# Kernel optimization log

Measured on AMD Instinct MI355X. Metric: run time of the kernel, lower is better.

Reference implementation:

```python
import jax, jax.numpy as jnp
import numpy as np

N = 50000
E = 400000
C_IN = 32
H = 64
RATIO = 0.5
SEQ_LEN = 5


def setup_inputs() -> dict:
    key = jax.random.key(0)
    ks = jax.random.split(key, 12)
    x = jax.random.normal(ks[0], (N, C_IN), jnp.float32)
    row = jax.random.randint(ks[1], (E,), 0, N, jnp.int32)
    off = jax.random.randint(ks[2], (E,), 1, N, jnp.int32)
    col = ((row + off) % N).astype(jnp.int32)  # no self-loops
    edge_index = jnp.stack([row, col])
    mask = jax.random.uniform(ks[3], (N,)) < 0.5

    def g(k, shape, fan):
        return jax.random.normal(k, shape, jnp.float32) / np.float32(np.sqrt(fan))

    return {
        "x": x, "edge_index": edge_index, "mask": mask,
        "conv0_w": g(ks[4], (C_IN, H), C_IN), "conv0_b": jnp.zeros((H,), jnp.float32),
        "conv1_w": g(ks[5], (H, H), H), "conv1_b": jnp.zeros((H,), jnp.float32),
        "pool_w": g(ks[6], (H,), H),
        "up_w": g(ks[7], (H, H), H), "up_b": jnp.zeros((H,), jnp.float32),
        "lstm0_w_ih": g(ks[8], (4 * H, H), H), "lstm0_w_hh": g(ks[9], (4 * H, H), H),
        "lstm0_b_ih": jnp.zeros((4 * H,), jnp.float32), "lstm0_b_hh": jnp.zeros((4 * H,), jnp.float32),
        "fin_w_ih": g(ks[10], (4 * H, H), H), "fin_w_hh": g(ks[11], (4 * H, H), H),
        "fin_b_ih": jnp.zeros((4 * H,), jnp.float32), "fin_b_hh": jnp.zeros((4 * H,), jnp.float32),
    }


def _coalesce(row, col, w, n):
    # sum duplicate (row, col) entries; output sorted by (row, col)
    key = row.astype(np.int64) * n + col.astype(np.int64)
    uk, inv = np.unique(key, return_inverse=True)
    w2 = np.bincount(inv, weights=w.astype(np.float64), minlength=uk.shape[0]).astype(np.float32)
    return uk // n, uk % n, w2


def _augment_adj(row, col, w, n):
    # remove self loops, add self loops (weight 1), compute A @ A (sparse), remove self loops
    m = row != col
    row = np.concatenate([row[m].astype(np.int64), np.arange(n, dtype=np.int64)])
    col = np.concatenate([col[m].astype(np.int64), np.arange(n, dtype=np.int64)])
    w = np.concatenate([w[m].astype(np.float32), np.ones(n, np.float32)])
    row, col, w = _coalesce(row, col, w, n)  # CSR-ordered
    cnt = np.bincount(row, minlength=n)
    indptr = np.concatenate([[0], np.cumsum(cnt)])
    dk = cnt[col]                      # out-degree of middle node k for each edge (i,k)
    starts = indptr[col]
    total = int(dk.sum())
    seg = np.repeat(np.cumsum(dk) - dk, dk)
    gi = np.repeat(starts, dk) + (np.arange(total) - seg)
    oi = np.repeat(row, dk)
    oj = col[gi]
    ow = np.repeat(w, dk) * w[gi]
    r2, c2, w2 = _coalesce(oi, oj, ow, n)
    m2 = r2 != c2
    return r2[m2], c2[m2], w2[m2]


def _gcn(x, row, col, ew, n, W, b):
    # GCNConv(improved=True): self-loop weight 2.0, symmetric deg^-1/2 normalization,
    # aggregate messages at target (col)
    h = x @ W
    loop = jnp.arange(n, dtype=row.dtype)
    r = jnp.concatenate([row, loop])
    c = jnp.concatenate([col, loop])
    w = jnp.concatenate([ew, jnp.full((n,), 2.0, ew.dtype)])
    deg = jax.ops.segment_sum(w, c, num_segments=n)
    dinv = jnp.where(deg > 0, jax.lax.rsqrt(deg), 0.0)
    norm = dinv[r] * w * dinv[c]
    out = jax.ops.segment_sum(norm[:, None] * h[r], c, num_segments=n)
    return out + b


def _sequences(x, mi):
    # sliding window [idx-L+1, idx] per masked node, zero left-padded
    t = mi[:, None] + jnp.arange(SEQ_LEN)[None, :] - (SEQ_LEN - 1)  # [M, L]
    return jnp.where((t >= 0)[:, :, None], x[jnp.clip(t, 0)], 0.0)


def _lstm_last(seq, w_ih, w_hh, b_ih, b_hh):
    # torch LSTM gate order: i, f, g, o; zero init state; return last hidden
    h = jnp.zeros((seq.shape[0], w_hh.shape[1]), seq.dtype)
    c = jnp.zeros_like(h)
    def step(carry, xt):
        h, c = carry
        g = xt @ w_ih.T + h @ w_hh.T + b_ih + b_hh
        i, f, gg, o = jnp.split(g, 4, axis=-1)
        c = jax.nn.sigmoid(f) * c + jax.nn.sigmoid(i) * jnp.tanh(gg)
        h = jax.nn.sigmoid(o) * jnp.tanh(c)
        return (h, c), None
    (h, _), _ = jax.lax.scan(step, (h, c), jnp.swapaxes(seq, 0, 1))
    return h


def reference(x, edge_index, mask, conv0_w, conv0_b, conv1_w, conv1_b, pool_w,
              up_w, up_b, lstm0_w_ih, lstm0_w_hh, lstm0_b_ih, lstm0_b_hh,
              fin_w_ih, fin_w_hh, fin_b_ih, fin_b_hh):
    n = x.shape[0]
    row0, col0 = edge_index[0], edge_index[1]
    ew0 = jnp.ones((row0.shape[0],), x.dtype)

    # down conv 0
    x1 = jax.nn.relu(_gcn(x, row0, col0, ew0, n, conv0_w, conv0_b))

    # augment_adj: sparse (A+I)^2 without diagonal (structural, constant)
    r2, c2, w2 = _augment_adj(np.asarray(row0), np.asarray(col0),
                              np.ones(row0.shape[0], np.float32), n)

    # TopKPooling: score = tanh((x.w)/||w||), keep top ceil(ratio*n)
    score = jnp.tanh((x1 @ pool_w) / jnp.linalg.norm(pool_w))
    k = int(np.ceil(RATIO * n))
    perm = np.argsort(-np.asarray(score), kind="stable")[:k]
    remap = np.full(n, -1, np.int64)
    remap[perm] = np.arange(k)
    keep = (remap[r2] >= 0) & (remap[c2] >= 0)
    pr = jnp.asarray(remap[r2[keep]].astype(np.int32))
    pc = jnp.asarray(remap[c2[keep]].astype(np.int32))
    pw = jnp.asarray(w2[keep])
    permj = jnp.asarray(perm.astype(np.int32))
    xp = x1[permj] * score[permj][:, None]

    # down conv 1 on pooled graph
    x2 = jax.nn.relu(_gcn(xp, pr, pc, pw, k, conv1_w, conv1_b))

    # up path (depth=1): LSTM over skip features at masked nodes
    mi = jnp.asarray(np.where(np.asarray(mask))[0].astype(np.int32))
    h0 = _lstm_last(_sequences(x1, mi), lstm0_w_ih, lstm0_w_hh, lstm0_b_ih, lstm0_b_hh)
    res = x1.at[mi].set(h0)
    up = jnp.zeros_like(x1).at[permj].set(x2)
    xo = _gcn(res + up, row0, col0, ew0, n, up_w, up_b)  # last level: no activation

    # final LSTM on masked nodes
    hf = _lstm_last(_sequences(xo, mi), fin_w_ih, fin_w_hh, fin_b_ih, fin_b_hh)
    return xo.at[mi].set(hf)
```

## Files before the change

### kernel.cpp

```cpp
#include <hip/hip_runtime.h>
#include <math.h>

#define NN 50000
#define EE 400000
#define CINV 32
#define KKEEP 25000
#define SEQL 5
#define HASH_BITS 20
#define HASH_SIZE (1u<<HASH_BITS)
#define HASH_MASK (HASH_SIZE-1u)
#define HEMPTY 0xFFFFFFFFu
#define PSB 196

typedef float vf4 __attribute__((ext_vector_type(4)));

__device__ __forceinline__ float sigm(float x){ return __builtin_amdgcn_rcpf(1.f+__expf(-x)); }
__device__ __forceinline__ float ftanh(float x){ return 1.f - 2.f*__builtin_amdgcn_rcpf(1.f+__expf(2.f*x)); }

__global__ void k_init(uint2* __restrict__ hash, unsigned* __restrict__ hist,
                       int* __restrict__ degcnt, int* __restrict__ diagint,
                       int* __restrict__ fillc,
                       unsigned* scal, unsigned long long* selp,
                       const float* __restrict__ w0, const float* __restrict__ b0i,
                       const float* __restrict__ b0h, const float* __restrict__ wf,
                       const float* __restrict__ bfi, const float* __restrict__ bfh,
                       float* __restrict__ WT0, float* __restrict__ WTf,
                       float* __restrict__ bs0, float* __restrict__ bsf){
  int i = blockIdx.x*256 + threadIdx.x;
  if (i < (int)HASH_SIZE) hash[i] = make_uint2(HEMPTY, 0u);
  if (i < 4*65536) hist[i] = 0u;
  if (i < NN){ degcnt[i]=0; diagint[i]=0; fillc[i]=0; }
  if (i < 256*64){
    int r = i>>6, k = i&63;
    int dst = k*256 + (r&63)*4 + (r>>6);
    WT0[dst] = w0[i];
    WTf[dst] = wf[i];
  }
  if (i < 256){
    int dst = (i&63)*4 + (i>>6);
    bs0[dst]=b0i[i]+b0h[i]; bsf[dst]=bfi[i]+bfh[i];
  }
  if (i == 0){ scal[0]=0u; scal[1]=0u; scal[3]=KKEEP; selp[0]=0ull; }
}

__global__ void k_phase2(const int* __restrict__ row, const int* __restrict__ col,
                         const int* __restrict__ mp, int* __restrict__ degcnt,
                         uint2* __restrict__ tab, unsigned* scal,
                         const float* __restrict__ X, const float* __restrict__ W,
                         float* __restrict__ Y){
  int idx = blockIdx.x*256 + threadIdx.x;
  if (idx < EE){
    int c = col[idx];
    atomicAdd(&degcnt[c], 1);
    unsigned key = (unsigned)row[idx]*50000u + (unsigned)c;
    unsigned h = (key*2654435761u) >> (32-HASH_BITS);
    for(;;){
      unsigned old = atomicCAS(&tab[h].x, HEMPTY, key);
      if (old==HEMPTY || old==key){ atomicAdd(&tab[h].y, 1u); break; }
      h = (h+1)&HASH_MASK;
    }
  }
  if (idx < NN/4){ if ((unsigned)mp[idx] > 1u) atomicOr(&scal[1], 1u); }
  if (idx < NN*16){
    int i = idx>>4, fq = idx&15;
    const vf4* X4 = (const vf4*)&X[i*CINV];
    const vf4* W4 = (const vf4*)W;
    vf4 acc = {0.f,0.f,0.f,0.f};
    #pragma unroll
    for (int kq=0;kq<CINV/4;kq++){
      vf4 xv = X4[kq];
      #pragma unroll
      for (int u=0;u<4;u++) acc += xv[u] * W4[(kq*4+u)*16+fq];
    }
    ((vf4*)Y)[i*16+fq] = acc;
  }
}

__global__ void k_psum1(const int* __restrict__ deg, const void* __restrict__ mp,
                        const unsigned* __restrict__ scal,
                        int* __restrict__ part, int* __restrict__ bsum,
                        int* __restrict__ mpart, int* __restrict__ mbsum,
                        float* __restrict__ dinv){
  __shared__ int sc[256];
  __shared__ int sm[256];
  int b = blockIdx.x, t = threadIdx.x, i = b*256+t;
  int v = (i<NN) ? deg[i] : 0;
  int mv = 0;
  if (i < NN){
    dinv[i] = rsqrtf((float)v + 2.0f);
    mv = scal[1] ? (int)(((const unsigned char*)mp)[i] != 0)
                 : (int)(((const int*)mp)[i] != 0);
  }
  sc[t] = v; sm[t] = mv; __syncthreads();
  for (int o=1;o<256;o<<=1){
    int x = (t>=o) ? sc[t-o] : 0;
    int y = (t>=o) ? sm[t-o] : 0;
    __syncthreads();
    sc[t] += x; sm[t] += y;
    __syncthreads();
  }
  if (i < NN){ part[i] = sc[t]-v; mpart[i] = sm[t]-mv; }
  if (t == 255){ bsum[b] = sc[255]; mbsum[b] = sm[255]; }
}
__global__ void k_psum3(const int* __restrict__ part, const int* __restrict__ bsum,
                        const int* __restrict__ mpart, const int* __restrict__ mbsum,
                        const void* __restrict__ mp, unsigned* __restrict__ scal,
                        int* __restrict__ indptr, int* __restrict__ mlist,
                        int* __restrict__ minv){
  __shared__ int sc[256];
  __shared__ int sm[256];
  int t = threadIdx.x;
  int v = (t<PSB) ? bsum[t] : 0;
  int w = (t<PSB) ? mbsum[t] : 0;
  sc[t] = v; sm[t] = w; __syncthreads();
  for (int o=1;o<256;o<<=1){
    int x = (t>=o) ? sc[t-o] : 0;
    int y = (t>=o) ? sm[t-o] : 0;
    __syncthreads();
    sc[t] += x; sm[t] += y;
    __syncthreads();
  }
  int bb = blockIdx.x;
  int ex  = sc[bb] - ((bb<PSB) ? bsum[bb] : 0);
  int mex = sm[bb] - ((bb<PSB) ? mbsum[bb] : 0);
  int i = bb*256 + t;
  if (i < NN){
    indptr[i] = part[i] + ex;
    int mv = scal[1] ? (int)(((const unsigned char*)mp)[i] != 0)
                     : (int)(((const int*)mp)[i] != 0);
    if (mv){ int p = mpart[i] + mex; mlist[p] = i; minv[i] = p; }
    else minv[i] = -1;
  }
  if (i == 0){ indptr[NN] = EE; scal[0] = (unsigned)sm[255]; }
}

__global__ void k_phase4(const int* __restrict__ row, const int* __restrict__ col,
                         const int* __restrict__ indptr, int* __restrict__ fillc,
                         int* __restrict__ csr_r, const uint2* __restrict__ tab,
                         int* __restrict__ diagint){
  int idx = blockIdx.x*256 + threadIdx.x;
  if (idx >= EE) return;
  int r = row[idx], c = col[idx];
  int pos = indptr[c] + atomicAdd(&fillc[c], 1);
  csr_r[pos] = r;
  unsigned rkey = (unsigned)c*50000u + (unsigned)r;
  unsigned h = (rkey*2654435761u) >> (32-HASH_BITS);
  for(;;){
    unsigned kk = tab[h].x;
    if (kk==rkey){ atomicAdd(&diagint[r], (int)tab[h].y); break; }
    if (kk==HEMPTY) break;
    h = (h+1)&HASH_MASK;
  }
}

__global__ void k_mm64v(const float* __restrict__ X, const float* __restrict__ W, float* __restrict__ Y){
  int idx = blockIdx.x*256 + threadIdx.x;
  if (idx >= NN*16) return;
  int i = idx>>4, fq = idx&15;
  const vf4* X4 = (const vf4*)&X[i*64];
  const vf4* W4 = (const vf4*)W;
  vf4 acc = {0.f,0.f,0.f,0.f};
  #pragma unroll
  for (int kq=0;kq<16;kq++){
    vf4 xv = X4[kq];
    #pragma unroll
    for (int u=0;u<4;u++) acc += xv[u] * W4[(kq*4+u)*16+fq];
  }
  ((vf4*)Y)[i*16+fq] = acc;
}

__global__ void g_gcn0(const int* __restrict__ indptr, const int* __restrict__ csr_r,
                       const float* __restrict__ dinv, const float* __restrict__ H,
                       const float* __restrict__ b, const float* __restrict__ pw,
                       float* __restrict__ out, unsigned long long* __restrict__ keys,
                       float* __restrict__ score, unsigned* __restrict__ hist){
  int node = blockIdx.x*4 + (threadIdx.x>>6), lane = threadIdx.x&63;
  if (node >= NN) return;
  int s = __builtin_amdgcn_readfirstlane(indptr[node]);
  int e = __builtin_amdgcn_readfirstlane(indptr[node+1]);
  int deg = e - s;
  float a0=0.f,a1=0.f,a2=0.f,a3=0.f,a4=0.f,a5=0.f,a6=0.f,a7=0.f;
  for (int base=0; base<deg; base+=64){
    int take = min(64, deg-base);
    bool act = lane < take;
    int ii = act ? csr_r[s+base+lane] : 0;
    float dv = act ? dinv[ii] : 0.f;
    for (int j=0; j<take; j+=8){
      int   r0=__shfl(ii,j,64),   r1=__shfl(ii,j+1,64), r2=__shfl(ii,j+2,64), r3=__shfl(ii,j+3,64),
            r4=__shfl(ii,j+4,64), r5=__shfl(ii,j+5,64), r6=__shfl(ii,j+6,64), r7=__shfl(ii,j+7,64);
      float d0=__shfl(dv,j,64),   d1=__shfl(dv,j+1,64), d2=__shfl(dv,j+2,64), d3=__shfl(dv,j+3,64),
            d4=__shfl(dv,j+4,64), d5=__shfl(dv,j+5,64), d6=__shfl(dv,j+6,64), d7=__shfl(dv,j+7,64);
      a0 += d0*H[(size_t)r0*64+lane];
      a1 += d1*H[(size_t)r1*64+lane];
      a2 += d2*H[(size_t)r2*64+lane];
      a3 += d3*H[(size_t)r3*64+lane];
      a4 += d4*H[(size_t)r4*64+lane];
      a5 += d5*H[(size_t)r5*64+lane];
      a6 += d6*H[(size_t)r6*64+lane];
      a7 += d7*H[(size_t)r7*64+lane];
    }
  }
  float acc = ((a0+a1)+(a2+a3)) + ((a4+a5)+(a6+a7));
  float di = dinv[node];
  float v = di*acc + 2.f*di*di*H[(size_t)node*64+lane] + b[lane];
  float x1v = fmaxf(v, 0.f);
  out[(size_t)node*64+lane] = x1v;
  float pv = pw[lane];
  float nq = pv*pv;
  float dq = x1v*pv;
  for (int o=32;o;o>>=1){ nq += __shfl_down(nq, o, 64); dq += __shfl_down(dq, o, 64); }
  if (lane==0){
    float sv = tanhf(dq / sqrtf(nq));
    sv = sv + 0.0f;
    score[node] = sv;
    unsigned u = __float_as_uint(sv);
    unsigned asc = (u>>31) ? ~u : (u | 0x80000000u);
    unsigned desc = ~asc;
    keys[node] = (((unsigned long long)desc)<<32) | (unsigned)node;
    atomicAdd(&hist[desc>>16], 1u);
  }
}
__global__ void g_t2(const int* __restrict__ indptr, const int* __restrict__ csr_r,
                     const float* __restrict__ dinv1, const float* __restrict__ hp,
                     float* __restrict__ t2){
  int node = blockIdx.x*4 + (threadIdx.x>>6), lane = threadIdx.x&63;
  if (node >= NN) return;
  int s = __builtin_amdgcn_readfirstlane(indptr[node]);
  int e = __builtin_amdgcn_readfirstlane(indptr[node+1]);
  int deg = e - s;
  float a0 = dinv1[node]*hp[(size_t)node*64+lane];
  float a1=0.f,a2=0.f,a3=0.f,a4=0.f,a5=0.f,a6=0.f,a7=0.f;
  for (int base=0; base<deg; base+=64){
    int take = min(64, deg-base);
    bool act = lane < take;
    int ii = act ? csr_r[s+base+lane] : 0;
    float dv = act ? dinv1[ii] : 0.f;
    for (int j=0; j<take; j+=8){
      int   r0=__shfl(ii,j,64),   r1=__shfl(ii,j+1,64), r2=__shfl(ii,j+2,64), r3=__shfl(ii,j+3,64),
            r4=__shfl(ii,j+4,64), r5=__shfl(ii,j+5,64), r6=__shfl(ii,j+6,64), r7=__shfl(ii,j+7,64);
      float d0=__shfl(dv,j,64),   d1=__shfl(dv,j+1,64), d2=__shfl(dv,j+2,64), d3=__shfl(dv,j+3,64),
            d4=__shfl(dv,j+4,64), d5=__shfl(dv,j+5,64), d6=__shfl(dv,j+6,64), d7=__shfl(dv,j+7,64);
      a0 += d0*hp[(size_t)r0*64+lane];
      a1 += d1*hp[(size_t)r1*64+lane];
      a2 += d2*hp[(size_t)r2*64+lane];
      a3 += d3*hp[(size_t)r3*64+lane];
      a4 += d4*hp[(size_t)r4*64+lane];
      a5 += d5*hp[(size_t)r5*64+lane];
      a6 += d6*hp[(size_t)r6*64+lane];
      a7 += d7*hp[(size_t)r7*64+lane];
    }
  }
  t2[(size_t)node*64+lane] = ((a0+a1)+(a2+a3)) + ((a4+a5)+(a6+a7));
}
__global__ void g_agg2y(const int* __restrict__ indptr, const int* __restrict__ csr_r,
                        const float* __restrict__ t2, const float* __restrict__ hp,
                        const float* __restrict__ dinv1, const int* __restrict__ diagint,
                        const int* __restrict__ kp, const float* __restrict__ b1,
                        const float* __restrict__ C, const float* __restrict__ Hbuf,
                        const int* __restrict__ minv, float* __restrict__ D){
  int node = blockIdx.x*4 + (threadIdx.x>>6), lane = threadIdx.x&63;
  if (node >= NN) return;
  int mv = minv[node];
  float base = (mv >= 0) ? Hbuf[(size_t)mv*64+lane] : C[(size_t)node*64+lane];
  float add = 0.f;
  if (kp[node]){
    int s = __builtin_amdgcn_readfirstlane(indptr[node]);
    int e = __builtin_amdgcn_readfirstlane(indptr[node+1]);
    int deg = e - s;
    float a0 = t2[(size_t)node*64+lane];
    float a1=0.f,a2=0.f,a3=0.f,a4=0.f,a5=0.f,a6=0.f,a7=0.f;
    for (int bs2=0; bs2<deg; bs2+=64){
      int take = min(64, deg-bs2);
      bool act = lane < take;
      int ii = act ? csr_r[s+bs2+lane] : 0;
      float wv = act ? 1.f : 0.f;
      for (int j=0; j<take; j+=8){
        int   r0=__shfl(ii,j,64),   r1=__shfl(ii,j+1,64), r2=__shfl(ii,j+2,64), r3=__shfl(ii,j+3,64),
              r4=__shfl(ii,j+4,64), r5=__shfl(ii,j+5,64), r6=__shfl(ii,j+6,64), r7=__shfl(ii,j+7,64);
        float w0=__shfl(wv,j,64),   w1=__shfl(wv,j+1,64), w2=__shfl(wv,j+2,64), w3=__shfl(wv,j+3,64),
              w4=__shfl(wv,j+4,64), w5=__shfl(wv,j+5,64), w6=__shfl(wv,j+6,64), w7=__shfl(wv,j+7,64);
        a0 += w0*t2[(size_t)r0*64+lane];
        a1 += w1*t2[(size_t)r1*64+lane];
        a2 += w2*t2[(size_t)r2*64+lane];
        a3 += w3*t2[(size_t)r3*64+lane];
        a4 += w4*t2[(size_t)r4*64+lane];
        a5 += w5*t2[(size_t)r5*64+lane];
        a6 += w6*t2[(size_t)r6*64+lane];
        a7 += w7*t2[(size_t)r7*64+lane];
      }
    }
    float acc = ((a0+a1)+(a2+a3)) + ((a4+a5)+(a6+a7));
    float di = dinv1[node], hv = hp[(size_t)node*64+lane];
    float diag = (float)(diagint[node] + 1);
    float v = di*(acc - diag*di*hv) + 2.f*di*di*hv + b1[lane];
    add = fmaxf(v, 0.f);
  }
  D[(size_t)node*64+lane] = base + add;
}
__global__ void g_up(const int* __restrict__ indptr, const int* __restrict__ csr_r,
                     const float* __restrict__ dinv, const float* __restrict__ H,
                     const float* __restrict__ b, float* __restrict__ xo, float* __restrict__ out){
  int node = blockIdx.x*4 + (threadIdx.x>>6), lane = threadIdx.x&63;
  if (node >= NN) return;
  int s = __builtin_amdgcn_readfirstlane(indptr[node]);
  int e = __builtin_amdgcn_readfirstlane(indptr[node+1]);
  int deg = e - s;
  float a0=0.f,a1=0.f,a2=0.f,a3=0.f,a4=0.f,a5=0.f,a6=0.f,a7=0.f;
  for (int base=0; base<deg; base+=64){
    int take = min(64, deg-base);
    bool act = lane < take;
    int ii = act ? csr_r[s+base+lane] : 0;
    float dv = act ? dinv[ii] : 0.f;
    for (int j=0; j<take; j+=8){
      int   r0=__shfl(ii,j,64),   r1=__shfl(ii,j+1,64), r2=__shfl(ii,j+2,64), r3=__shfl(ii,j+3,64),
            r4=__shfl(ii,j+4,64), r5=__shfl(ii,j+5,64), r6=__shfl(ii,j+6,64), r7=__shfl(ii,j+7,64);
      float d0=__shfl(dv,j,64),   d1=__shfl(dv,j+1,64), d2=__shfl(dv,j+2,64), d3=__shfl(dv,j+3,64),
            d4=__shfl(dv,j+4,64), d5=__shfl(dv,j+5,64), d6=__shfl(dv,j+6,64), d7=__shfl(dv,j+7,64);
      a0 += d0*H[(size_t)r0*64+lane];
      a1 += d1*H[(size_t)r1*64+lane];
      a2 += d2*H[(size_t)r2*64+lane];
      a3 += d3*H[(size_t)r3*64+lane];
      a4 += d4*H[(size_t)r4*64+lane];
      a5 += d5*H[(size_t)r5*64+lane];
      a6 += d6*H[(size_t)r6*64+lane];
      a7 += d7*H[(size_t)r7*64+lane];
    }
  }
  float acc = ((a0+a1)+(a2+a3)) + ((a4+a5)+(a6+a7));
  float di = dinv[node];
  float v = di*acc + 2.f*di*di*H[(size_t)node*64+lane] + b[lane];
  xo[(size_t)node*64+lane] = v; out[(size_t)node*64+lane] = v;
}

__global__ void k_hist(const unsigned long long* __restrict__ keys, unsigned* __restrict__ hist,
                       const unsigned long long* __restrict__ selp, int round){
  int i = blockIdx.x*256 + threadIdx.x;
  if (i >= NN) return;
  unsigned long long key = keys[i];
  int shift = 48 - 16*round;
  if ((key>>(shift+16)) == selp[0])
    atomicAdd(&hist[(unsigned)((key>>shift)&0xFFFFull)], 1u);
}
__global__ void k_pick(const unsigned* __restrict__ hist, unsigned long long* selp, unsigned* scal){
  __shared__ unsigned csum[256];
  __shared__ unsigned bins[256];
  __shared__ int schunk;
  int t = threadIdx.x;
  const uint4* h4 = (const uint4*)(hist + t*256);
  unsigned s = 0;
  #pragma unroll 8
  for (int j=0;j<64;j++){ uint4 v = h4[j]; s += v.x+v.y+v.z+v.w; }
  csum[t] = s;
  __syncthreads();
  if (t==0){
    unsigned rem = scal[3];
    int chunk = 255;
    for (int c2=0;c2<256;c2++){ unsigned cc=csum[c2]; if (rem>cc) rem-=cc; else { chunk=c2; break; } }
    schunk = chunk; scal[3] = rem;
  }
  __syncthreads();
  bins[t] = hist[schunk*256 + t];
  __syncthreads();
  if (t==0){
    unsigned rem = scal[3];
    int bin = schunk*256 + 255;
    for (int b=0;b<256;b++){ unsigned hv=bins[b]; if (rem>hv) rem-=hv; else { bin = schunk*256 + b; break; } }
    selp[0] = (selp[0]<<16) | (unsigned long long)(unsigned)bin;
    scal[3] = rem;
  }
}
__global__ void k_tsg(const int* __restrict__ indptr, const int* __restrict__ csr_r,
                      const unsigned long long* __restrict__ keys,
                      const unsigned long long* __restrict__ selp,
                      int* __restrict__ kp, int* __restrict__ ts){
  int i = blockIdx.x*256 + threadIdx.x;
  if (i >= NN) return;
  unsigned long long sp = selp[0];
  int s = indptr[i], e = indptr[i+1];
  int self = (keys[i] <= sp) ? 1 : 0;
  kp[i] = self;
  int acc = self;
  for (int j=s;j<e;j++) acc += (keys[csr_r[j]] <= sp) ? 1 : 0;
  ts[i] = acc;
}
__global__ void k_csgmm(const int* __restrict__ indptr, const int* __restrict__ csr_r,
                        const int* __restrict__ ts, const int* __restrict__ diagint,
                        const int* __restrict__ kp, float* __restrict__ dinv1,
                        const float* __restrict__ X, const float* __restrict__ W,
                        const float* __restrict__ sc, float* __restrict__ Y){
  int idx = blockIdx.x*256 + threadIdx.x;
  if (idx < NN*16){
    int i = idx>>4, fq = idx&15;
    if (!kp[i]){ vf4 z = {0.f,0.f,0.f,0.f}; ((vf4*)Y)[i*16+fq] = z; return; }
    const vf4* X4 = (const vf4*)&X[i*64];
    const vf4* W4 = (const vf4*)W;
    vf4 acc = {0.f,0.f,0.f,0.f};
    #pragma unroll
    for (int kq=0;kq<16;kq++){
      vf4 xv = X4[kq];
      #pragma unroll
      for (int u=0;u<4;u++) acc += xv[u] * W4[(kq*4+u)*16+fq];
    }
    acc *= sc[i];
    ((vf4*)Y)[i*16+fq] = acc;
  } else {
    int i = idx - NN*16;
    if (i >= NN) return;
    int s = indptr[i], e = indptr[i+1];
    int acc = ts[i];
    for (int j=s;j<e;j++) acc += ts[csr_r[j]];
    dinv1[i] = kp[i] ? rsqrtf((float)(acc - diagint[i] - 1) + 2.0f) : 0.f;
  }
}

__global__ __launch_bounds__(256) void k_xw(const float* __restrict__ src,
        const float* __restrict__ WT, const float* __restrict__ bsum,
        float* __restrict__ XW){
  __shared__ vf4 Wl[4096];
  int t = threadIdx.x;
  const vf4* Wg = (const vf4*)WT;
  for (int u=t; u<4096; u+=256) Wl[u] = Wg[u];
  int fq = t & 63, wv = t >> 6;
  vf4 bias = ((const vf4*)bsum)[fq];
  __syncthreads();
  for (int g = blockIdx.x*4 + wv; g < NN/4; g += gridDim.x*4){
    int n0 = g*4;
    const vf4* X4 = (const vf4*)&src[(size_t)n0*64];
    vf4 a0=bias, a1=bias, a2=bias, a3=bias;
    #pragma unroll 4
    for (int kq=0;kq<16;kq++){
      vf4 x0 = X4[kq], x1 = X4[16+kq], x2 = X4[32+kq], x3 = X4[48+kq];
      vf4 w0 = Wl[(kq*4+0)*64+fq];
      vf4 w1 = Wl[(kq*4+1)*64+fq];
      vf4 w2 = Wl[(kq*4+2)*64+fq];
      vf4 w3 = Wl[(kq*4+3)*64+fq];
      a0 += x0.x*w0 + x0.y*w1 + x0.z*w2 + x0.w*w3;
      a1 += x1.x*w0 + x1.y*w1 + x1.z*w2 + x1.w*w3;
      a2 += x2.x*w0 + x2.y*w1 + x2.z*w2 + x2.w*w3;
      a3 += x3.x*w0 + x3.y*w1 + x3.z*w2 + x3.w*w3;
    }
    vf4* Y = (vf4*)XW;
    Y[(size_t)n0*64 + fq]       = a0;
    Y[(size_t)n0*64 + 64 + fq]  = a1;
    Y[(size_t)n0*64 + 128 + fq] = a2;
    Y[(size_t)n0*64 + 192 + fq] = a3;
  }
}

__global__ __launch_bounds__(256) void k_rec(const float* __restrict__ XW,
        const float* __restrict__ whh, const float* __restrict__ bsum,
        const int* __restrict__ mlist, const unsigned* __restrict__ scal,
        float* __restrict__ dst, int scatter){
  int M = (int)scal[0];
  if (M < 0 || M > NN) M = 0;
  int task = blockIdx.x;
  if (task*4 >= M) return;
  int w = threadIdx.x>>6, lane = threadIdx.x&63;
  int r = w*64 + lane;
  const vf4* g4 = (const vf4*)&whh[(size_t)r*64];
  vf4 wh[16];
  #pragma unroll
  for (int j=0;j<16;j++) wh[j] = g4[j];
  __shared__ float sh[4][64];
  __shared__ float gates[4][4][64];
  int m = task*4 + w;
  bool valid = (m < M);
  int node = mlist[valid ? m : (M-1)];
  node = min(max(node, 0), NN-1);
  const vf4* XW4 = (const vf4*)XW;
  vf4 bp = ((const vf4*)bsum)[lane];
  vf4 xs0, xs1, xs2, xs3, xs4;
  {
    int r0 = node - 4, r1 = node - 3;
    xs0 = (r0 >= 0) ? XW4[(size_t)r0*64 + lane] : bp;
    xs1 = (r1 >= 0) ? XW4[(size_t)r1*64 + lane] : bp;
  }
  float c, h;
  c = sigm(xs0.x)*ftanh(xs0.z);
  h = sigm(xs0.w)*ftanh(c);
  sh[w][lane] = h;
  __syncthreads();
  #pragma unroll
  for (int t=1;t<SEQL;t++){
    if (t==1){ int ri = node-2; xs2 = (ri>=0) ? XW4[(size_t)ri*64+lane] : bp; }
    if (t==2){ int ri = node-1; xs3 = (ri>=0) ? XW4[(size_t)ri*64+lane] : bp; }
    if (t==3){ xs4 = XW4[(size_t)node*64 + lane]; }
    vf4 a0={0,0,0,0}, a1={0,0,0,0}, a2={0,0,0,0}, a3={0,0,0,0};
    #pragma unroll
    for (int j=0;j<16;j++){
      vf4 wj = wh[j];
      a0 += (*(const vf4*)&sh[0][j*4]) * wj;
      a1 += (*(const vf4*)&sh[1][j*4]) * wj;
      a2 += (*(const vf4*)&sh[2][j*4]) * wj;
      a3 += (*(const vf4*)&sh[3][j*4]) * wj;
    }
    gates[0][w][lane] = a0.x+a0.y+a0.z+a0.w;
    gates[1][w][lane] = a1.x+a1.y+a1.z+a1.w;
    gates[2][w][lane] = a2.x+a2.y+a2.z+a2.w;
    gates[3][w][lane] = a3.x+a3.y+a3.z+a3.w;
    __syncthreads();
    vf4 xv = (t==1) ? xs1 : (t==2) ? xs2 : (t==3) ? xs3 : xs4;
    float gi = gates[w][0][lane] + xv.x;
    float gf = gates[w][1][lane] + xv.y;
    float gg = gates[w][2][lane] + xv.z;
    float go = gates[w][3][lane] + xv.w;
    c = sigm(gf)*c + sigm(gi)*ftanh(gg);
    h = sigm(go)*ftanh(c);
    sh[w][lane] = h;
    __syncthreads();
  }
  if (valid){
    size_t o = scatter ? ((size_t)node*64 + lane) : ((size_t)m*64 + lane);
    dst[o] = h;
  }
}

extern "C" void kernel_launch(void* const* d_in, const int* in_sizes, int n_in,
                              void* d_out, int out_size, void* d_ws, size_t ws_size,
                              hipStream_t stream) {
  const float* x   = (const float*)d_in[0];
  const int*   ei  = (const int*)d_in[1];
  const int*   row = ei;
  const int*   col = ei + EE;
  const void*  mp  = d_in[2];
  const float* W0  = (const float*)d_in[3];
  const float* b0  = (const float*)d_in[4];
  const float* W1  = (const float*)d_in[5];
  const float* b1  = (const float*)d_in[6];
  const float* pw  = (const float*)d_in[7];
  const float* Wu  = (const float*)d_in[8];
  const float* bu  = (const float*)d_in[9];
  const float* l0wih=(const float*)d_in[10];
  const float* l0whh=(const float*)d_in[11];
  const float* l0bih=(const float*)d_in[12];
  const float* l0bhh=(const float*)d_in[13];
  const float* lfwih=(const float*)d_in[14];
  const float* lfwhh=(const float*)d_in[15];
  const float* lfbih=(const float*)d_in[16];
  const float* lfbhh=(const float*)d_in[17];

  char* wp = (char*)d_ws;
  auto alloc = [&](size_t bytes)->char*{ char* p = wp; wp += ((bytes+255)/256)*256; return p; };
  float* A     = (float*)alloc((size_t)NN*64*4);
  float* B     = (float*)alloc((size_t)NN*64*4);
  float* C     = (float*)alloc((size_t)NN*64*4);
  float* D     = (float*)alloc((size_t)NN*64*4);
  float* Ebuf  = (float*)alloc((size_t)NN*64*4);
  float* Hbuf  = (float*)alloc((size_t)NN*64*4);
  float* XW    = (float*)alloc((size_t)NN*256*4);
  float* WT0   = (float*)alloc((size_t)256*64*4);
  float* WTf   = (float*)alloc((size_t)256*64*4);
  float* bs0   = (float*)alloc((size_t)256*4);
  float* bsf   = (float*)alloc((size_t)256*4);
  float* score = (float*)alloc((size_t)NN*4);
  float* dinv0 = (float*)alloc((size_t)NN*4);
  float* dinv1 = (float*)alloc((size_t)NN*4);
  unsigned long long* keys = (unsigned long long*)alloc((size_t)NN*8);
  int* degcnt  = (int*)alloc((size_t)NN*4);
  int* diagint = (int*)alloc((size_t)NN*4);
  int* ts      = (int*)alloc((size_t)NN*4);
  int* kp      = (int*)alloc((size_t)NN*4);
  int* mlist   = (int*)alloc((size_t)NN*4);
  int* minv    = (int*)alloc((size_t)NN*4);
  int* indptr  = (int*)alloc((size_t)(NN+1)*4);
  int* part    = (int*)alloc((size_t)NN*4);
  int* mpart   = (int*)alloc((size_t)NN*4);
  int* fillc   = (int*)alloc((size_t)NN*4);
  int* bsum    = (int*)alloc((size_t)256*4);
  int* mbsum   = (int*)alloc((size_t)256*4);
  int* csr_r   = (int*)alloc((size_t)EE*4);
  uint2* hash  = (uint2*)alloc((size_t)HASH_SIZE*8);
  unsigned* hist=(unsigned*)alloc((size_t)4*65536*4);
  unsigned* scal=(unsigned*)alloc(256);
  unsigned long long* selp = (unsigned long long*)(scal + 4);

  #define GRID1(n) dim3(((n)+255)/256), dim3(256), 0, stream
  #define GRIDW dim3((NN+3)/4), dim3(256), 0, stream

  k_init<<<GRID1(HASH_SIZE)>>>(hash, hist, degcnt, diagint, fillc,
                               scal, selp, l0wih, l0bih, l0bhh, lfwih, lfbih, lfbhh,
                               WT0, WTf, bs0, bsf);
  k_phase2<<<GRID1(NN*16)>>>(row, col, (const int*)mp, degcnt, hash, scal, x, W0, A);
  k_psum1<<<dim3(PSB),dim3(256),0,stream>>>(degcnt, mp, scal, part, bsum, mpart, mbsum, dinv0);
  k_psum3<<<dim3(PSB),dim3(256),0,stream>>>(part, bsum, mpart, mbsum, mp, scal, indptr, mlist, minv);
  k_phase4<<<GRID1(EE)>>>(row, col, indptr, fillc, csr_r, hash, diagint);

  g_gcn0<<<GRIDW>>>(indptr, csr_r, dinv0, A, b0, pw, C, keys, score, hist);

  k_pick<<<dim3(1),dim3(256),0,stream>>>(hist, selp, scal);
  for (int r2=1;r2<4;r2++){
    k_hist<<<GRID1(NN)>>>(keys, hist + r2*65536, selp, r2);
    k_pick<<<dim3(1),dim3(256),0,stream>>>(hist + r2*65536, selp, scal);
  }
  k_tsg<<<GRID1(NN)>>>(indptr, csr_r, keys, selp, kp, ts);
  k_csgmm<<<GRID1(NN*16+NN)>>>(indptr, csr_r, ts, diagint, kp, dinv1, C, W1, score, Ebuf);
  g_t2<<<GRIDW>>>(indptr, csr_r, dinv1, Ebuf, A);

  k_xw<<<dim3(512),dim3(256),0,stream>>>(C, WT0, bs0, XW);
  k_rec<<<dim3(12500),dim3(256),0,stream>>>(XW, l0whh, bs0, mlist, scal, Hbuf, 0);

  g_agg2y<<<GRIDW>>>(indptr, csr_r, A, Ebuf, dinv1, diagint, kp, b1, C, Hbuf, minv, D);

  k_mm64v<<<GRID1(NN*16)>>>(D, Wu, Ebuf);
  g_up<<<GRIDW>>>(indptr, csr_r, dinv0, Ebuf, bu, B, (float*)d_out);

  k_xw<<<dim3(512),dim3(256),0,stream>>>(B, WTf, bsf, XW);
  k_rec<<<dim3(12500),dim3(256),0,stream>>>(XW, lfwhh, bsf, mlist, scal, (float*)d_out, 1);
  #undef GRIDW
  #undef GRID1
}
```

Before: 642.0 us.

## Restructure LSTM recurrence to one node per two-wave block with double-buffered gates

The LSTM recurrence kernel moves from four nodes per 256-thread block (one gate row per thread) to one node per 128-thread block. Each wave now holds two gate rows (32 vf4 registers) and recomputes the cell state redundantly, so each wave only ever reads its own hidden state. Gate results are double-buffered in shared memory, which removes the second barrier per timestep. The aim is shorter per-step critical paths and fewer barriers. The cost is that recurrent weights are reloaded per node instead of per four nodes, register pressure is higher, and four times as many blocks are launched.

```diff
diff --git a/kernel.cpp b/kernel.cpp
--- a/kernel.cpp
+++ b/kernel.cpp
@@ -447,25 +447,23 @@
   }
 }
 
-__global__ __launch_bounds__(256) void k_rec(const float* __restrict__ XW,
+__global__ __launch_bounds__(128) void k_rec(const float* __restrict__ XW,
         const float* __restrict__ whh, const float* __restrict__ bsum,
         const int* __restrict__ mlist, const unsigned* __restrict__ scal,
         float* __restrict__ dst, int scatter){
   int M = (int)scal[0];
   if (M < 0 || M > NN) M = 0;
   int task = blockIdx.x;
-  if (task*4 >= M) return;
+  if (task >= M) return;
   int w = threadIdx.x>>6, lane = threadIdx.x&63;
-  int r = w*64 + lane;
-  const vf4* g4 = (const vf4*)&whh[(size_t)r*64];
-  vf4 wh[16];
+  const vf4* gA = (const vf4*)&whh[(size_t)((2*w+0)*64+lane)*64];
+  const vf4* gB = (const vf4*)&whh[(size_t)((2*w+1)*64+lane)*64];
+  vf4 wh[32];
   #pragma unroll
-  for (int j=0;j<16;j++) wh[j] = g4[j];
-  __shared__ float sh[4][64];
-  __shared__ float gates[4][4][64];
-  int m = task*4 + w;
-  bool valid = (m < M);
-  int node = mlist[valid ? m : (M-1)];
+  for (int j=0;j<16;j++){ wh[j] = gA[j]; wh[16+j] = gB[j]; }
+  __shared__ __align__(16) float shh[2][64];
+  __shared__ float gx[2][4][64];
+  int node = mlist[task];
   node = min(max(node, 0), NN-1);
   const vf4* XW4 = (const vf4*)XW;
   vf4 bp = ((const vf4*)bsum)[lane];
@@ -475,42 +473,38 @@
     xs0 = (r0 >= 0) ? XW4[(size_t)r0*64 + lane] : bp;
     xs1 = (r1 >= 0) ? XW4[(size_t)r1*64 + lane] : bp;
   }
-  float c, h;
-  c = sigm(xs0.x)*ftanh(xs0.z);
-  h = sigm(xs0.w)*ftanh(c);
-  sh[w][lane] = h;
-  __syncthreads();
+  float c = sigm(xs0.x)*ftanh(xs0.z);
+  float h = sigm(xs0.w)*ftanh(c);
+  shh[w][lane] = h;
   #pragma unroll
   for (int t=1;t<SEQL;t++){
     if (t==1){ int ri = node-2; xs2 = (ri>=0) ? XW4[(size_t)ri*64+lane] : bp; }
     if (t==2){ int ri = node-1; xs3 = (ri>=0) ? XW4[(size_t)ri*64+lane] : bp; }
     if (t==3){ xs4 = XW4[(size_t)node*64 + lane]; }
-    vf4 a0={0,0,0,0}, a1={0,0,0,0}, a2={0,0,0,0}, a3={0,0,0,0};
+    asm volatile("s_waitcnt lgkmcnt(0)" ::: "memory");
+    __builtin_amdgcn_sched_barrier(0);
+    vf4 aA={0,0,0,0}, aB={0,0,0,0};
     #pragma unroll
     for (int j=0;j<16;j++){
-      vf4 wj = wh[j];
-      a0 += (*(const vf4*)&sh[0][j*4]) * wj;
-      a1 += (*(const vf4*)&sh[1][j*4]) * wj;
-      a2 += (*(const vf4*)&sh[2][j*4]) * wj;
-      a3 += (*(const vf4*)&sh[3][j*4]) * wj;
-    }
-    gates[0][w][lane] = a0.x+a0.y+a0.z+a0.w;
-    gates[1][w][lane] = a1.x+a1.y+a1.z+a1.w;
-    gates[2][w][lane] = a2.x+a2.y+a2.z+a2.w;
-    gates[3][w][lane] = a3.x+a3.y+a3.z+a3.w;
+      vf4 hv = *(const vf4*)&shh[w][j*4];
+      aA += hv*wh[j];
+      aB += hv*wh[16+j];
+    }
+    int pb = t & 1;
+    gx[pb][2*w+0][lane] = aA.x+aA.y+aA.z+aA.w;
+    gx[pb][2*w+1][lane] = aB.x+aB.y+aB.z+aB.w;
     __syncthreads();
     vf4 xv = (t==1) ? xs1 : (t==2) ? xs2 : (t==3) ? xs3 : xs4;
-    float gi = gates[w][0][lane] + xv.x;
-    float gf = gates[w][1][lane] + xv.y;
-    float gg = gates[w][2][lane] + xv.z;
-    float go = gates[w][3][lane] + xv.w;
+    float gi = gx[pb][0][lane] + xv.x;
+    float gf = gx[pb][1][lane] + xv.y;
+    float gg = gx[pb][2][lane] + xv.z;
+    float go = gx[pb][3][lane] + xv.w;
     c = sigm(gf)*c + sigm(gi)*ftanh(gg);
     h = sigm(go)*ftanh(c);
-    sh[w][lane] = h;
-    __syncthreads();
-  }
-  if (valid){
-    size_t o = scatter ? ((size_t)node*64 + lane) : ((size_t)m*64 + lane);
+    if (t < SEQL-1) shh[w][lane] = h;
+  }
+  if (w == 0){
+    size_t o = scatter ? ((size_t)node*64 + lane) : ((size_t)task*64 + lane);
     dst[o] = h;
   }
 }
@@ -597,7 +591,7 @@
   g_t2<<<GRIDW>>>(indptr, csr_r, dinv1, Ebuf, A);
 
   k_xw<<<dim3(512),dim3(256),0,stream>>>(C, WT0, bs0, XW);
-  k_rec<<<dim3(12500),dim3(256),0,stream>>>(XW, l0whh, bs0, mlist, scal, Hbuf, 0);
+  k_rec<<<dim3(NN),dim3(128),0,stream>>>(XW, l0whh, bs0, mlist, scal, Hbuf, 0);
 
   g_agg2y<<<GRIDW>>>(indptr, csr_r, A, Ebuf, dinv1, diagint, kp, b1, C, Hbuf, minv, D);
 
@@ -605,7 +599,7 @@
   g_up<<<GRIDW>>>(indptr, csr_r, dinv0, Ebuf, bu, B, (float*)d_out);
 
   k_xw<<<dim3(512),dim3(256),0,stream>>>(B, WTf, bsf, XW);
-  k_rec<<<dim3(12500),dim3(256),0,stream>>>(XW, lfwhh, bsf, mlist, scal, (float*)d_out, 1);
+  k_rec<<<dim3(NN),dim3(128),0,stream>>>(XW, lfwhh, bsf, mlist, scal, (float*)d_out, 1);
   #undef GRIDW
   #undef GRID1
 }
```

After: 873.9 us. 36.1% more time.
